# Optimization experiments

Hardware: AMD Instinct MI355X
Metric: run time of the kernel (lower is better)

Reference implementation:

```python
import jax, jax.numpy as jnp
import numpy as np

B, NBC, H, W, HID, OUT = 4, 128, 64, 64, 64, 1
NINT = H * W

def _lin_init(key, fan_in, fan_out):
    kw, kb = jax.random.split(key)
    bound = 1.0 / np.sqrt(fan_in)
    w = jax.random.uniform(kw, (fan_in, fan_out), minval=-bound, maxval=bound, dtype=jnp.float32)
    b = jax.random.uniform(kb, (fan_out,), minval=-bound, maxval=bound, dtype=jnp.float32)
    return w, b

def setup_inputs() -> dict:
    key = jax.random.key(0)
    ks = jax.random.split(key, 7)
    boundary_info = jax.random.normal(ks[0], (B, NBC, 3), dtype=jnp.float32)
    interior_coords = jax.random.uniform(ks[1], (B, NINT, 2), minval=-1.0, maxval=1.0, dtype=jnp.float32)
    W0, b0 = _lin_init(ks[2], 3, HID)        # boundary_encoder layer 0
    W1, b1 = _lin_init(ks[3], HID, HID)      # boundary_encoder layer 1
    G0w, G0b = _lin_init(ks[4], HID + 2, HID)  # green_kernel layer 0
    G1w, G1b = _lin_init(ks[5], HID, HID)      # green_kernel layer 1
    G2w, G2b = _lin_init(ks[6], HID, OUT)      # green_kernel layer 2
    return {"boundary_info": boundary_info, "interior_coords": interior_coords,
            "W0": W0, "b0": b0, "W1": W1, "b1": b1,
            "G0w": G0w, "G0b": G0b, "G1w": G1w, "G1b": G1b,
            "G2w": G2w, "G2b": G2b,
            "interior_h": H, "interior_w": W}

def reference(boundary_info, interior_coords, W0, b0, W1, b1,
              G0w, G0b, G1w, G1b, G2w, G2b, interior_h, interior_w):
    batch, n_bc, _ = boundary_info.shape
    hid = W0.shape[1]
    # boundary encoder: (B, NBC, HID)
    bf = jax.nn.relu(boundary_info @ W0 + b0)
    bf = jax.nn.relu(bf @ W1 + b1)
    # green kernel layer 0: split weight over concat([bf, coords]) so the
    # concatenated (B,NBC,NINT,HID+2) tensor is never materialized.
    a = bf @ G0w[:hid]                      # (B, NBC, HID)
    c = interior_coords @ G0w[hid:]         # (B, NINT, HID)
    h1 = jax.nn.relu(a[:, :, None, :] + c[:, None, :, :] + G0b)  # (B,NBC,NINT,HID)
    h2 = jax.nn.relu(h1 @ G1w + G1b)        # (B, NBC, NINT, HID)
    contribution = h2 @ G2w + G2b           # (B, NBC, NINT, OUT)
    u = contribution.sum(axis=1) / n_bc     # (B, NINT, OUT)
    return u.reshape(batch, 1, interior_h, interior_w)
```

## Files before the change

kernel.cpp:

```cpp
#include <hip/hip_runtime.h>

#define BB   4
#define NBC  128
#define NINT 4096
#define HID  64

using half8   = __attribute__((ext_vector_type(8)))  _Float16;
using h2      = __attribute__((ext_vector_type(2)))  _Float16;
using float16 = __attribute__((ext_vector_type(16))) float;
using f2      = __attribute__((ext_vector_type(2)))  float;
using int4v   = __attribute__((ext_vector_type(4)))  int;

static __device__ __forceinline__ h2 cvt_pkrtz(float a, float b) {
#if __has_builtin(__builtin_amdgcn_cvt_pkrtz)
    return __builtin_bit_cast(h2, __builtin_amdgcn_cvt_pkrtz(a, b));
#else
    h2 r;
    asm("v_cvt_pkrtz_f16_f32 %0, %1, %2" : "=v"(r) : "v"(a), "v"(b));
    return r;
#endif
}

__global__ void __launch_bounds__(256) bge_prep(
    const float* __restrict__ binfo,
    const float* __restrict__ W0,
    const float* __restrict__ b0,
    const float* __restrict__ W1,
    const float* __restrict__ b1,
    const float* __restrict__ G0w,
    const float* __restrict__ G0b,
    float* __restrict__ aprime)
{
    __shared__ float sW1[HID * HID];
    __shared__ float sG0[HID * HID];
    __shared__ float shv [4][HID];
    __shared__ float shv2[4][HID];

    const int tid = threadIdx.x;
    const int wv  = tid >> 6;
    const int t   = tid & 63;
    const int row = blockIdx.x * 4 + wv;

    for (int idx = tid; idx < HID * HID / 4; idx += 256) {
        ((float4*)sW1)[idx] = ((const float4*)W1)[idx];
        ((float4*)sG0)[idx] = ((const float4*)G0w)[idx];
    }

    const float x0 = binfo[row*3+0];
    const float x1 = binfo[row*3+1];
    const float x2 = binfo[row*3+2];
    float h = fmaxf(x0*W0[t] + x1*W0[64+t] + x2*W0[128+t] + b0[t], 0.0f);
    shv[wv][t] = h;
    __syncthreads();

    float acc = b1[t];
    #pragma unroll 8
    for (int k = 0; k < HID; ++k) acc += shv[wv][k] * sW1[k*64 + t];
    shv2[wv][t] = fmaxf(acc, 0.0f);
    __syncthreads();

    float a = G0b[t];
    #pragma unroll 8
    for (int k = 0; k < HID; ++k) a += shv2[wv][k] * sG0[k*64 + t];
    aprime[row*HID + t] = a;
}

__global__ void __launch_bounds__(512) bge_main(
    const float* __restrict__ icoord,
    const float* __restrict__ G0w,
    const float* __restrict__ G1w,
    const float* __restrict__ G1b,
    const float* __restrict__ G2w,
    const float* __restrict__ G2b,
    const float* __restrict__ aprime,
    float* __restrict__ out)
{
    __shared__ __align__(16) float smem[65*HID + 256];
    float* const ldsA = smem;
    float* const red  = smem + 65*HID;

    const int b    = blockIdx.y >> 1;
    const int bch  = blockIdx.y & 1;
    const int i0   = blockIdx.x * 32;
    const int tid  = threadIdx.x;
    const int wv   = tid >> 6;
    const int lane = tid & 63;
    const int hf   = lane >> 5;
    const int ln   = lane & 31;

    {
        const float4* src = (const float4*)(aprime + ((size_t)b * NBC + bch*64) * HID);
        float4* dst = (float4*)ldsA;
        for (int idx = tid; idx < 64*HID/4; idx += 512) dst[idx] = src[idx];
    }

    const int i = i0 + ln;
    const float cx = icoord[((size_t)b*NINT + i)*2 + 0];
    const float cy = icoord[((size_t)b*NINT + i)*2 + 1];
    f2 cre2[4][4];
    #pragma unroll
    for (int st = 0; st < 4; ++st)
        #pragma unroll
        for (int j = 0; j < 4; ++j) {
            const int k = st*16 + hf*8 + 2*j;
            f2 t;
            t[0] = cx*G0w[64*64 + k]     + cy*G0w[65*64 + k];
            t[1] = cx*G0w[64*64 + k + 1] + cy*G0w[65*64 + k + 1];
            cre2[st][j] = t;
        }

    half8 bfrag[4][2];
    #pragma unroll
    for (int st = 0; st < 4; ++st)
        #pragma unroll
        for (int t = 0; t < 2; ++t)
            #pragma unroll
            for (int jj = 0; jj < 8; ++jj) {
                const int k = st*16 + hf*8 + jj;
                bfrag[st][t][jj] = (_Float16)(G1w[k*64 + t*32 + ln]);
            }

    const float b1v0 = G1b[ln],  b1v1 = G1b[32 + ln];
    const float g2v0 = G2w[ln],  g2v1 = G2w[32 + ln];
    const float g2bv = G2b[0];

    f2 bb; bb[0] = b1v0; bb[1] = b1v1;
    h2 g2pk; g2pk[0] = (_Float16)g2v0; g2pk[1] = (_Float16)g2v1;

    h2 z2; z2[0] = (_Float16)0.0f; z2[1] = (_Float16)0.0f;
    const float16 zc = (float16)0.0f;
    float s[16];
    #pragma unroll
    for (int r = 0; r < 16; ++r) s[r] = 0.0f;

    __syncthreads();

    const int bc0 = wv * 8;

    #define BUILD_AFS(DST, AROW)                                               \
        {                                                                      \
            const float* arow_ = (AROW);                                       \
            _Pragma("unroll")                                                  \
            for (int st = 0; st < 4; ++st) {                                   \
                const float4* ap4 = (const float4*)(arow_ + st*16 + hf*8);     \
                const float4 v0 = ap4[0], v1 = ap4[1];                         \
                f2 p0, p1, p2, p3;                                             \
                p0[0] = v0.x; p0[1] = v0.y;                                    \
                p1[0] = v0.z; p1[1] = v0.w;                                    \
                p2[0] = v1.x; p2[1] = v1.y;                                    \
                p3[0] = v1.z; p3[1] = v1.w;                                    \
                p0 += cre2[st][0];                                             \
                p1 += cre2[st][1];                                             \
                p2 += cre2[st][2];                                             \
                p3 += cre2[st][3];                                             \
                h2 c0 = cvt_pkrtz(p0[0], p0[1]);                               \
                h2 c1 = cvt_pkrtz(p1[0], p1[1]);                               \
                h2 c2 = cvt_pkrtz(p2[0], p2[1]);                               \
                h2 c3 = cvt_pkrtz(p3[0], p3[1]);                               \
                c0 = __builtin_elementwise_max(c0, z2);                        \
                c1 = __builtin_elementwise_max(c1, z2);                        \
                c2 = __builtin_elementwise_max(c2, z2);                        \
                c3 = __builtin_elementwise_max(c3, z2);                        \
                int4v di;                                                      \
                di[0] = __builtin_bit_cast(int, c0);                           \
                di[1] = __builtin_bit_cast(int, c1);                           \
                di[2] = __builtin_bit_cast(int, c2);                           \
                di[3] = __builtin_bit_cast(int, c3);                           \
                DST[st] = __builtin_bit_cast(half8, di);                       \
            }                                                                  \
        }

    half8 afs[4];
    BUILD_AFS(afs, ldsA + bc0*HID);

    #pragma unroll 4
    for (int j = 0; j < 8; ++j) {
        float16 acc0 = __builtin_amdgcn_mfma_f32_32x32x16_f16(afs[0], bfrag[0][0], zc, 0, 0, 0);
        float16 acc1 = __builtin_amdgcn_mfma_f32_32x32x16_f16(afs[0], bfrag[0][1], zc, 0, 0, 0);
        acc0 = __builtin_amdgcn_mfma_f32_32x32x16_f16(afs[1], bfrag[1][0], acc0, 0, 0, 0);
        acc1 = __builtin_amdgcn_mfma_f32_32x32x16_f16(afs[1], bfrag[1][1], acc1, 0, 0, 0);
        acc0 = __builtin_amdgcn_mfma_f32_32x32x16_f16(afs[2], bfrag[2][0], acc0, 0, 0, 0);
        acc1 = __builtin_amdgcn_mfma_f32_32x32x16_f16(afs[2], bfrag[2][1], acc1, 0, 0, 0);
        acc0 = __builtin_amdgcn_mfma_f32_32x32x16_f16(afs[3], bfrag[3][0], acc0, 0, 0, 0);
        acc1 = __builtin_amdgcn_mfma_f32_32x32x16_f16(afs[3], bfrag[3][1], acc1, 0, 0, 0);

        half8 afn[4];
        BUILD_AFS(afn, ldsA + (bc0 + j + 1)*HID);

        #pragma unroll
        for (int r = 0; r < 16; ++r) {
            f2 y; y[0] = acc0[r]; y[1] = acc1[r];
            y += bb;
            h2 hp = cvt_pkrtz(y[0], y[1]);
            hp = __builtin_elementwise_max(hp, z2);
#if __has_builtin(__builtin_amdgcn_fdot2)
            s[r] = __builtin_amdgcn_fdot2(hp, g2pk, s[r], false);
#else
            s[r] += (float)hp[0]*(float)g2pk[0] + (float)hp[1]*(float)g2pk[1];
#endif
        }

        afs[0] = afn[0]; afs[1] = afn[1]; afs[2] = afn[2]; afs[3] = afn[3];
    }
    #undef BUILD_AFS

    #pragma unroll
    for (int r = 0; r < 16; ++r) {
        float v = s[r];
        v += __shfl_xor(v, 1);
        v += __shfl_xor(v, 2);
        v += __shfl_xor(v, 4);
        v += __shfl_xor(v, 8);
        v += __shfl_xor(v, 16);
        s[r] = v;
    }
    if (ln == 0) {
        #pragma unroll
        for (int r = 0; r < 16; ++r) red[wv*32 + hf*16 + r] = s[r];
    }
    __syncthreads();

    if (tid < 32) {
        const int m   = tid;
        const int h_m = (m >> 2) & 1;
        const int r_m = (m & 3) | ((m >> 3) << 2);
        float acc = 0.0f;
        #pragma unroll
        for (int w = 0; w < 8; ++w) acc += red[w*32 + h_m*16 + r_m];
        atomicAdd(out + (size_t)b*NINT + i0 + m, acc * (1.0f/128.0f) + g2bv * 0.5f);
    }
}

extern "C" void kernel_launch(void* const* d_in, const int* in_sizes, int n_in,
                              void* d_out, int out_size, void* d_ws, size_t ws_size,
                              hipStream_t stream) {
    const float* binfo  = (const float*)d_in[0];
    const float* icoord = (const float*)d_in[1];
    const float* W0     = (const float*)d_in[2];
    const float* b0     = (const float*)d_in[3];
    const float* W1     = (const float*)d_in[4];
    const float* b1     = (const float*)d_in[5];
    const float* G0w    = (const float*)d_in[6];
    const float* G0b    = (const float*)d_in[7];
    const float* G1w    = (const float*)d_in[8];
    const float* G1b    = (const float*)d_in[9];
    const float* G2w    = (const float*)d_in[10];
    const float* G2b    = (const float*)d_in[11];

    float* aprime = (float*)d_ws;

    hipMemsetAsync(d_out, 0, (size_t)BB * NINT * sizeof(float), stream);

    hipLaunchKernelGGL(bge_prep, dim3(BB*NBC/4), dim3(256), 0, stream,
                       binfo, W0, b0, W1, b1, G0w, G0b, aprime);
    hipLaunchKernelGGL(bge_main, dim3(NINT/32, BB*2), dim3(512), 0, stream,
                       icoord, G0w, G1w, G1b, G2w, G2b, aprime,
                       (float*)d_out);
}
```

Measured before the change: 127.4 us.

## Give each block all boundary points, fold bias into MFMA, pipeline LDS loads

Each block now covers all 128 boundary conditions for its 32 interior points, not half of them. That lets it write the output directly, so the memset and the atomic adds are no longer needed. The G1 bias is preloaded into the MFMA accumulator, which removes a vector add per element. Raw LDS rows are double-buffered in registers so the fp32→fp16 conversion can interleave with the MFMAs, and s_setprio hints are placed around the MFMAs. The grid is halved and LDS use roughly doubles, which reduces parallelism and may lower occupancy.

```diff
diff --git a/kernel.cpp b/kernel.cpp
--- a/kernel.cpp
+++ b/kernel.cpp
@@ -75,12 +75,11 @@
     const float* __restrict__ aprime,
     float* __restrict__ out)
 {
-    __shared__ __align__(16) float smem[65*HID + 256];
+    __shared__ __align__(16) float smem[(NBC + 1)*HID + 256];
     float* const ldsA = smem;
-    float* const red  = smem + 65*HID;
-
-    const int b    = blockIdx.y >> 1;
-    const int bch  = blockIdx.y & 1;
+    float* const red  = smem + (NBC + 1)*HID;
+
+    const int b    = blockIdx.y;
     const int i0   = blockIdx.x * 32;
     const int tid  = threadIdx.x;
     const int wv   = tid >> 6;
@@ -89,9 +88,9 @@
     const int ln   = lane & 31;
 
     {
-        const float4* src = (const float4*)(aprime + ((size_t)b * NBC + bch*64) * HID);
+        const float4* src = (const float4*)(aprime + (size_t)b * NBC * HID);
         float4* dst = (float4*)ldsA;
-        for (int idx = tid; idx < 64*HID/4; idx += 512) dst[idx] = src[idx];
+        for (int idx = tid; idx < NBC*HID/4; idx += 512) dst[idx] = src[idx];
     }
 
     const int i = i0 + ln;
@@ -124,32 +123,43 @@
     const float g2v0 = G2w[ln],  g2v1 = G2w[32 + ln];
     const float g2bv = G2b[0];
 
-    f2 bb; bb[0] = b1v0; bb[1] = b1v1;
+    float16 cb0, cb1;
+    #pragma unroll
+    for (int r = 0; r < 16; ++r) { cb0[r] = b1v0; cb1[r] = b1v1; }
+
     h2 g2pk; g2pk[0] = (_Float16)g2v0; g2pk[1] = (_Float16)g2v1;
 
     h2 z2; z2[0] = (_Float16)0.0f; z2[1] = (_Float16)0.0f;
-    const float16 zc = (float16)0.0f;
     float s[16];
     #pragma unroll
     for (int r = 0; r < 16; ++r) s[r] = 0.0f;
 
     __syncthreads();
 
-    const int bc0 = wv * 8;
-
-    #define BUILD_AFS(DST, AROW)                                               \
+    const int bc0 = wv * 16;
+
+    #define LOADROW(DST, ROW)                                                  \
         {                                                                      \
-            const float* arow_ = (AROW);                                       \
+            const float4* ap_ = (const float4*)(ldsA + (ROW)*HID) + hf*2;      \
+            _Pragma("unroll")                                                  \
+            for (int st_ = 0; st_ < 4; ++st_) {                                \
+                DST[2*st_]   = ap_[st_*4];                                     \
+                DST[2*st_+1] = ap_[st_*4 + 1];                                 \
+            }                                                                  \
+        }
+
+    #define BODY(SRC)                                                          \
+        {                                                                      \
+            float16 acc0, acc1;                                                \
             _Pragma("unroll")                                                  \
             for (int st = 0; st < 4; ++st) {                                   \
-                const float4* ap4 = (const float4*)(arow_ + st*16 + hf*8);     \
-                const float4 v0 = ap4[0], v1 = ap4[1];                         \
+                const float4 v0 = SRC[2*st], v1 = SRC[2*st+1];                 \
                 f2 p0, p1, p2, p3;                                             \
                 p0[0] = v0.x; p0[1] = v0.y;                                    \
                 p1[0] = v0.z; p1[1] = v0.w;                                    \
                 p2[0] = v1.x; p2[1] = v1.y;                                    \
                 p3[0] = v1.z; p3[1] = v1.w;                                    \
-                p0 += cre2[st][0];                                             \
+                p0 += cre2[st][0];            \
                 p1 += cre2[st][1];                                             \
                 p2 += cre2[st][2];                                             \
                 p3 += cre2[st][3];                                             \
@@ -166,43 +176,35 @@
                 di[1] = __builtin_bit_cast(int, c1);                           \
                 di[2] = __builtin_bit_cast(int, c2);                           \
                 di[3] = __builtin_bit_cast(int, c3);                           \
-                DST[st] = __builtin_bit_cast(half8, di);                       \
+                const half8 af = __builtin_bit_cast(half8, di);                \
+                __builtin_amdgcn_s_setprio(1);                                 \
+                if (st == 0) {                                                 \
+                    acc0 = __builtin_amdgcn_mfma_f32_32x32x16_f16(af, bfrag[0][0], cb0, 0, 0, 0); \
+                    acc1 = __builtin_amdgcn_mfma_f32_32x32x16_f16(af, bfrag[0][1], cb1, 0, 0, 0); \
+                } else {                                                       \
+                    acc0 = __builtin_amdgcn_mfma_f32_32x32x16_f16(af, bfrag[st][0], acc0, 0, 0, 0); \
+                    acc1 = __builtin_amdgcn_mfma_f32_32x32x16_f16(af, bfrag[st][1], acc1, 0, 0, 0); \
+                }                                                              \
+                __builtin_amdgcn_s_setprio(0);                                 \
+            }                                                                  \
+            _Pragma("unroll")                                                  \
+            for (int r = 0; r < 16; ++r) {                                     \
+                h2 hp = cvt_pkrtz(acc0[r], acc1[r]);                           \
+                hp = __builtin_elementwise_max(hp, z2);                        \
+                s[r] = __builtin_amdgcn_fdot2(hp, g2pk, s[r], false);          \
             }                                                                  \
         }
 
-    half8 afs[4];
-    BUILD_AFS(afs, ldsA + bc0*HID);
-
-    #pragma unroll 4
-    for (int j = 0; j < 8; ++j) {
-        float16 acc0 = __builtin_amdgcn_mfma_f32_32x32x16_f16(afs[0], bfrag[0][0], zc, 0, 0, 0);
-        float16 acc1 = __builtin_amdgcn_mfma_f32_32x32x16_f16(afs[0], bfrag[0][1], zc, 0, 0, 0);
-        acc0 = __builtin_amdgcn_mfma_f32_32x32x16_f16(afs[1], bfrag[1][0], acc0, 0, 0, 0);
-        acc1 = __builtin_amdgcn_mfma_f32_32x32x16_f16(afs[1], bfrag[1][1], acc1, 0, 0, 0);
-        acc0 = __builtin_amdgcn_mfma_f32_32x32x16_f16(afs[2], bfrag[2][0], acc0, 0, 0, 0);
-        acc1 = __builtin_amdgcn_mfma_f32_32x32x16_f16(afs[2], bfrag[2][1], acc1, 0, 0, 0);
-        acc0 = __builtin_amdgcn_mfma_f32_32x32x16_f16(afs[3], bfrag[3][0], acc0, 0, 0, 0);
-        acc1 = __builtin_amdgcn_mfma_f32_32x32x16_f16(afs[3], bfrag[3][1], acc1, 0, 0, 0);
-
-        half8 afn[4];
-        BUILD_AFS(afn, ldsA + (bc0 + j + 1)*HID);
-
-        #pragma unroll
-        for (int r = 0; r < 16; ++r) {
-            f2 y; y[0] = acc0[r]; y[1] = acc1[r];
-            y += bb;
-            h2 hp = cvt_pkrtz(y[0], y[1]);
-            hp = __builtin_elementwise_max(hp, z2);
-#if __has_builtin(__builtin_amdgcn_fdot2)
-            s[r] = __builtin_amdgcn_fdot2(hp, g2pk, s[r], false);
-#else
-            s[r] += (float)hp[0]*(float)g2pk[0] + (float)hp[1]*(float)g2pk[1];
-#endif
-        }
-
-        afs[0] = afn[0]; afs[1] = afn[1]; afs[2] = afn[2]; afs[3] = afn[3];
-    }
-    #undef BUILD_AFS
+    float4 ldA[8], ldB[8];
+    LOADROW(ldA, bc0);
+    for (int jj = 0; jj < 8; ++jj) {
+        LOADROW(ldB, bc0 + 2*jj + 1);
+        BODY(ldA);
+        LOADROW(ldA, bc0 + 2*jj + 2);
+        BODY(ldB);
+    }
+    #undef LOADROW
+    #undef BODY
 
     #pragma unroll
     for (int r = 0; r < 16; ++r) {
@@ -227,7 +229,7 @@
         float acc = 0.0f;
         #pragma unroll
         for (int w = 0; w < 8; ++w) acc += red[w*32 + h_m*16 + r_m];
-        atomicAdd(out + (size_t)b*NINT + i0 + m, acc * (1.0f/128.0f) + g2bv * 0.5f);
+        out[(size_t)b*NINT + i0 + m] = acc * (1.0f/128.0f) + g2bv;
     }
 }
 
@@ -249,11 +251,9 @@
 
     float* aprime = (float*)d_ws;
 
-    hipMemsetAsync(d_out, 0, (size_t)BB * NINT * sizeof(float), stream);
-
     hipLaunchKernelGGL(bge_prep, dim3(BB*NBC/4), dim3(256), 0, stream,
                        binfo, W0, b0, W1, b1, G0w, G0b, aprime);
-    hipLaunchKernelGGL(bge_main, dim3(NINT/32, BB*2), dim3(512), 0, stream,
+    hipLaunchKernelGGL(bge_main, dim3(NINT/32, BB), dim3(512), 0, stream,
                        icoord, G0w, G1w, G1b, G2w, G2b, aprime,
                        (float*)d_out);
 }
```

Result: faster. 113.8 us (-10.7%).
